# Optimization experiments

Hardware: AMD Instinct MI355X
Metric: run time of the kernel (lower is better)

The kernel has to match this reference:

```python
import jax, jax.numpy as jnp
import numpy as np

N, D_IN, D_K = 8192, 512, 64


def setup_inputs() -> dict:
    key = jax.random.key(0)
    k0, k1, k2, k3 = jax.random.split(key, 4)
    return {
        "inputs": jax.random.normal(k0, (N, D_IN), dtype=jnp.float32),
        "Wq": jax.random.normal(k1, (D_K, D_IN), dtype=jnp.float32),
        "Wk": jax.random.normal(k2, (D_K, D_IN), dtype=jnp.float32),
        "Wv": jax.random.normal(k3, (D_K, D_IN), dtype=jnp.float32),
    }


def reference(inputs, Wq, Wk, Wv):
    # nn.Linear(bias=False): x @ W.T, W has shape [out, in]
    q = inputs @ Wq.T  # [N, Dk]
    k = inputs @ Wk.T  # [N, Dk]
    v = inputs @ Wv.T  # [N, Dk]
    scaled = (q @ k.T) / jnp.sqrt(jnp.float32(D_K))  # [N, N]
    attn = jax.nn.softmax(scaled, axis=1)            # softmax over keys (dim=1)
    # weighted = values[:,None] * attn.T[:,:,None]; sum over dim 0 == attn @ v
    return attn @ v  # [N, Dk]
```

## Files before the change

### kernel.cpp

```cpp
#include <hip/hip_runtime.h>
#include <hip/hip_bf16.h>


#define N_TOK 8192
#define D_INN 512
#define DK    64

typedef __attribute__((ext_vector_type(8))) short bf16x8;
typedef __attribute__((ext_vector_type(4))) float f32x4;

#define GLOAD_LDS16(gsrc, ldst) \
  __builtin_amdgcn_global_load_lds( \
      (const __attribute__((address_space(1))) unsigned int*)(gsrc), \
      (__attribute__((address_space(3))) unsigned int*)(ldst), 16, 0, 0)

static __device__ __forceinline__ unsigned f2bf_u(float f) {
  union { float f; unsigned u; } v; v.f = f;
  return (v.u + 0x7FFFu + ((v.u >> 16) & 1u)) >> 16;
}
static __device__ __forceinline__ unsigned short f2bf(float f) { return (unsigned short)f2bf_u(f); }
static __device__ __forceinline__ float bf2f(unsigned short h) {
  union { unsigned u; float f; } v; v.u = ((unsigned)h) << 16; return v.f;
}
static __device__ __forceinline__ unsigned truncpk(float a, float b) {
  union { float f; unsigned u; } x, y; x.f = a; y.f = b;
  return (x.u >> 16) | (y.u & 0xFFFF0000u);
}
static __device__ __forceinline__ void split2(float a, float b, unsigned& hi, unsigned& lo) {
  unsigned ha = f2bf_u(a), hb = f2bf_u(b);
  float ra = a - bf2f((unsigned short)ha);
  float rb = b - bf2f((unsigned short)hb);
  hi = ha | (hb << 16);
  lo = f2bf_u(ra) | (f2bf_u(rb) << 16);
}
static __device__ __forceinline__ void split8(const float* p, bf16x8& hi, bf16x8& lo) {
  float4 a = *(const float4*)p;
  float4 b = *(const float4*)(p + 4);
  union { unsigned u[4]; bf16x8 v; } H, L;
  split2(a.x, a.y, H.u[0], L.u[0]);
  split2(a.z, a.w, H.u[1], L.u[1]);
  split2(b.x, b.y, H.u[2], L.u[2]);
  split2(b.z, b.w, H.u[3], L.u[3]);
  hi = H.v; lo = L.v;
}
static __device__ __forceinline__ bf16x8 round8(const float* p) {
  float4 a = *(const float4*)p;
  float4 b = *(const float4*)(p + 4);
  union { unsigned u[4]; bf16x8 v; } H;
  H.u[0] = f2bf_u(a.x) | (f2bf_u(a.y) << 16);
  H.u[1] = f2bf_u(a.z) | (f2bf_u(a.w) << 16);
  H.u[2] = f2bf_u(b.x) | (f2bf_u(b.y) << 16);
  H.u[3] = f2bf_u(b.z) | (f2bf_u(b.w) << 16);
  return H.v;
}

__global__ __launch_bounds__(256, 2) void qkv3(
    const float* __restrict__ X,
    const float* __restrict__ Wq, const float* __restrict__ Wk, const float* __restrict__ Wv,
    unsigned short* __restrict__ qhp, unsigned short* __restrict__ qlp,
    unsigned short* __restrict__ kph, unsigned short* __restrict__ kpl,
    unsigned short* __restrict__ vp) {
  const int tid = threadIdx.x, w = tid >> 6, l = tid & 63;
  const int l15 = l & 15, g = l >> 4;
  const int t0 = blockIdx.x * 16;
  const int dq = w * 16;

  f32x4 aq = {0.f, 0.f, 0.f, 0.f}, ak = aq, av = aq;

  for (int kc = 0; kc < D_INN; kc += 32) {
    bf16x8 ah, al;
    split8(X + (t0 + l15) * D_INN + kc + g * 8, ah, al);

    const int woff = (dq + l15) * D_INN + kc + g * 8;
    bf16x8 bqh, bql, bkh, bkl;
    split8(Wq + woff, bqh, bql);
    split8(Wk + woff, bkh, bkl);
    bf16x8 bvh = round8(Wv + woff);

    aq = __builtin_amdgcn_mfma_f32_16x16x32_bf16(ah, bqh, aq, 0, 0, 0);
    aq = __builtin_amdgcn_mfma_f32_16x16x32_bf16(ah, bql, aq, 0, 0, 0);
    aq = __builtin_amdgcn_mfma_f32_16x16x32_bf16(al, bqh, aq, 0, 0, 0);
    ak = __builtin_amdgcn_mfma_f32_16x16x32_bf16(ah, bkh, ak, 0, 0, 0);
    ak = __builtin_amdgcn_mfma_f32_16x16x32_bf16(ah, bkl, ak, 0, 0, 0);
    ak = __builtin_amdgcn_mfma_f32_16x16x32_bf16(al, bkh, ak, 0, 0, 0);
    av = __builtin_amdgcn_mfma_f32_16x16x32_bf16(ah, bvh, av, 0, 0, 0);
    av = __builtin_amdgcn_mfma_f32_16x16x32_bf16(al, bvh, av, 0, 0, 0);
  }

#pragma unroll
  for (int r = 0; r < 4; r++) {
    float v = aq[r] * 0.125f;
    int row = t0 + g * 4 + r;
    unsigned short h = f2bf(v);
    qhp[row * DK + dq + l15] = h;
    qlp[row * DK + dq + l15] = f2bf(v - bf2f(h));
  }
#pragma unroll
  for (int r = 0; r < 4; r++) {
    float v = ak[r];
    int t = t0 + g * 4 + r;
    int d = dq + l15;
    int off = (t >> 5) * 2048 + ((t >> 4) & 1) * 1024 + (d >> 5) * 512 +
              ((t & 15) + (((d >> 3) & 3) << 4)) * 8 + (d & 7);
    unsigned short h = f2bf(v);
    kph[off] = h;
    kpl[off] = f2bf(v - bf2f(h));
  }
  {
    int tg = t0 + g * 4;
    int d = dq + l15;
    int off = (tg >> 5) * 2048 + (d >> 4) * 512 +
              (((d & 15) + (((tg >> 3) & 3) << 4))) * 8 + (tg & 7);
    uint2 pk;
    pk.x = f2bf_u(av[0]) | (f2bf_u(av[1]) << 16);
    pk.y = f2bf_u(av[2]) | (f2bf_u(av[3]) << 16);
    *(uint2*)(vp + off) = pk;
  }
}

static __device__ __forceinline__ void stage_tile(
    const unsigned short* __restrict__ kph, const unsigned short* __restrict__ kpl,
    const unsigned short* __restrict__ vp, int kti,
    unsigned short* lds, int w, int l) {
  const unsigned short* kb = kph + kti * 2048;
  const unsigned short* lb = kpl + kti * 2048;
  const unsigned short* vb = vp + kti * 2048;
#pragma unroll
  for (int j = 0; j < 6; ++j) {
    int chunk = w * 6 + j;
    const unsigned short* src = (chunk < 8) ? kb : ((chunk < 16) ? lb : vb);
    GLOAD_LDS16(src + (chunk & 7) * 512 + l * 8, lds + chunk * 512);
  }
}

__global__ __launch_bounds__(256, 2) void attn5(
    const unsigned short* __restrict__ qhp, const unsigned short* __restrict__ qlp,
    const unsigned short* __restrict__ kph, const unsigned short* __restrict__ kpl,
    const unsigned short* __restrict__ vp,
    unsigned short* __restrict__ pnb, float* __restrict__ pden, float* __restrict__ pM) {
  __shared__ unsigned short kv_lds[2 * 12288];
  __shared__ unsigned short P_lds[4 * 16 * 72];

  const int tid = threadIdx.x, w = tid >> 6, l = tid & 63;
  const int l15 = l & 15, g = l >> 4;
  const int qblk = blockIdx.x >> 4, ks = blockIdx.x & 15;
  const int wq0 = qblk * 128 + w * 32;

  bf16x8 qhf[2][2], qlf[2][2];
#pragma unroll
  for (int u = 0; u < 2; u++)
#pragma unroll
    for (int c = 0; c < 2; c++) {
      int row = wq0 + u * 16 + l15;
      qhf[u][c] = *(const bf16x8*)(qhp + row * DK + c * 32 + g * 8);
      qlf[u][c] = *(const bf16x8*)(qlp + row * DK + c * 32 + g * 8);
    }

  const short onec = (short)0x3F80;
  const bf16x8 ones = {onec, onec, onec, onec, onec, onec, onec, onec};

  f32x4 accO[2][4], accL[2];
  float m[2] = {-1e30f, -1e30f};
#pragma unroll
  for (int u = 0; u < 2; u++) {
    accL[u] = f32x4{0.f, 0.f, 0.f, 0.f};
#pragma unroll
    for (int ds = 0; ds < 4; ds++) accO[u][ds] = f32x4{0.f, 0.f, 0.f, 0.f};
  }

  const int kti0 = ks * 16;
  stage_tile(kph, kpl, vp, kti0, kv_lds, w, l);
  __syncthreads();

  for (int t = 0; t < 8; ++t) {
    const int cb = (t & 1) ? 12288 : 0;
    const int pb = 12288 - cb;
    const int ktin = (t < 7) ? (kti0 + 2 * t + 2) : (kti0 + 2 * t);
    stage_tile(kph, kpl, vp, ktin, kv_lds + pb, w, l);

    const unsigned short* Kh = kv_lds + cb;
    const unsigned short* Kl = Kh + 4096;
    const unsigned short* Vv = Kh + 8192;

    f32x4 st[2][4];
#pragma unroll
    for (int s = 0; s < 4; s++) {
      bf16x8 khf[2], klf[2];
#pragma unroll
      for (int c = 0; c < 2; c++) {
        const int off = (s >> 1) * 2048 + (s & 1) * 1024 + c * 512 + l * 8;
        khf[c] = *(const bf16x8*)(Kh + off);
        klf[c] = *(const bf16x8*)(Kl + off);
      }
      __builtin_amdgcn_s_setprio(1);
#pragma unroll
      for (int u = 0; u < 2; u++) {
        f32x4 sa = {0.f, 0.f, 0.f, 0.f};
        sa = __builtin_amdgcn_mfma_f32_16x16x32_bf16(khf[0], qhf[u][0], sa, 0, 0, 0);
        sa = __builtin_amdgcn_mfma_f32_16x16x32_bf16(khf[1], qhf[u][1], sa, 0, 0, 0);
        sa = __builtin_amdgcn_mfma_f32_16x16x32_bf16(khf[0], qlf[u][0], sa, 0, 0, 0);
        sa = __builtin_amdgcn_mfma_f32_16x16x32_bf16(khf[1], qlf[u][1], sa, 0, 0, 0);
        sa = __builtin_amdgcn_mfma_f32_16x16x32_bf16(klf[0], qhf[u][0], sa, 0, 0, 0);
        sa = __builtin_amdgcn_mfma_f32_16x16x32_bf16(klf[1], qhf[u][1], sa, 0, 0, 0);
        st[u][s] = sa;
      }
      __builtin_amdgcn_s_setprio(0);
    }

    bf16x8 pa[2][2];
#pragma unroll
    for (int u = 0; u < 2; u++) {
      float t0m = fmaxf(fmaxf(st[u][0][0], st[u][0][1]), fmaxf(st[u][0][2], st[u][0][3]));
      float t1m = fmaxf(fmaxf(st[u][1][0], st[u][1][1]), fmaxf(st[u][1][2], st[u][1][3]));
      float t2m = fmaxf(fmaxf(st[u][2][0], st[u][2][1]), fmaxf(st[u][2][2], st[u][2][3]));
      float t3m = fmaxf(fmaxf(st[u][3][0], st[u][3][1]), fmaxf(st[u][3][2], st[u][3][3]));
      float tm = fmaxf(fmaxf(t0m, t1m), fmaxf(t2m, t3m));
      tm = fmaxf(tm, __shfl_xor(tm, 16, 64));
      tm = fmaxf(tm, __shfl_xor(tm, 32, 64));
      if (__any(tm > m[u] + 8.f)) {
        float mn = fmaxf(m[u], tm);
        float fac = __expf(m[u] - mn);
        m[u] = mn;
#pragma unroll
        for (int r = 0; r < 4; r++) {
          float fr = __shfl(fac, g * 4 + r, 64);
          accL[u][r] *= fr;
#pragma unroll
          for (int ds = 0; ds < 4; ds++) accO[u][ds][r] *= fr;
        }
      }
      const int base = (w * 16 + l15) * 72;
#pragma unroll
      for (int s = 0; s < 4; s++) {
        float p0 = __expf(st[u][s][0] - m[u]);
        float p1 = __expf(st[u][s][1] - m[u]);
        float p2 = __expf(st[u][s][2] - m[u]);
        float p3 = __expf(st[u][s][3] - m[u]);
        *(unsigned*)&P_lds[base + s * 16 + g * 4]     = truncpk(p0, p1);
        *(unsigned*)&P_lds[base + s * 16 + g * 4 + 2] = truncpk(p2, p3);
      }
#pragma unroll
      for (int c = 0; c < 2; c++)
        pa[u][c] = *(const bf16x8*)&P_lds[base + c * 32 + g * 8];
      accL[u] = __builtin_amdgcn_mfma_f32_16x16x32_bf16(pa[u][0], ones, accL[u], 0, 0, 0);
      accL[u] = __builtin_amdgcn_mfma_f32_16x16x32_bf16(pa[u][1], ones, accL[u], 0, 0, 0);
    }

    __builtin_amdgcn_s_setprio(1);
#pragma unroll
    for (int ds = 0; ds < 4; ds++) {
      bf16x8 vb[2];
#pragma unroll
      for (int c = 0; c < 2; c++)
        vb[c] = *(const bf16x8*)(Vv + c * 2048 + ds * 512 + l * 8);
#pragma unroll
      for (int u = 0; u < 2; u++) {
        accO[u][ds] = __builtin_amdgcn_mfma_f32_16x16x32_bf16(pa[u][0], vb[0], accO[u][ds], 0, 0, 0);
        accO[u][ds] = __builtin_amdgcn_mfma_f32_16x16x32_bf16(pa[u][1], vb[1], accO[u][ds], 0, 0, 0);
      }
    }
    __builtin_amdgcn_s_setprio(0);

    __syncthreads();
  }

#pragma unroll
  for (int u = 0; u < 2; u++) {
#pragma unroll
    for (int ds = 0; ds < 4; ds++)
#pragma unroll
      for (int r = 0; r < 4; r++)
        pnb[(size_t)ks * (N_TOK * DK) + (wq0 + u * 16 + g * 4 + r) * DK + ds * 16 + l15] =
            f2bf(accO[u][ds][r]);
    if (l15 == 0) {
#pragma unroll
      for (int r = 0; r < 4; r++) pden[ks * N_TOK + wq0 + u * 16 + g * 4 + r] = accL[u][r];
    }
    if (g == 0) pM[ks * N_TOK + wq0 + u * 16 + l15] = m[u];
  }
}

__global__ __launch_bounds__(256) void merge16(
    const unsigned short* __restrict__ pnb, const float* __restrict__ pden,
    const float* __restrict__ pM, float* __restrict__ out) {
  int i = blockIdx.x * 256 + threadIdx.x;
  int q = i >> 6, d = i & 63;
  float M = -1e30f;
#pragma unroll
  for (int s = 0; s < 16; s++) M = fmaxf(M, pM[s * N_TOK + q]);
  float num = 0.f, den = 0.f;
#pragma unroll
  for (int s = 0; s < 16; s++) {
    float e = __expf(pM[s * N_TOK + q] - M);
    num += bf2f(pnb[(size_t)s * (N_TOK * DK) + q * DK + d]) * e;
    den += pden[s * N_TOK + q] * e;
  }
  out[i] = num / den;
}

extern "C" void kernel_launch(void* const* d_in, const int* in_sizes, int n_in,
                              void* d_out, int out_size, void* d_ws, size_t ws_size,
                              hipStream_t stream) {
  (void)in_sizes; (void)n_in; (void)out_size; (void)ws_size;
  const float* X  = (const float*)d_in[0];
  const float* Wq = (const float*)d_in[1];
  const float* Wk = (const float*)d_in[2];
  const float* Wv = (const float*)d_in[3];

  char* base = (char*)d_ws;
  unsigned short* pnb = (unsigned short*)(base);
  unsigned short* qhp = (unsigned short*)(base + 16777216);
  unsigned short* qlp = (unsigned short*)(base + 17825792);
  unsigned short* kph = (unsigned short*)(base + 18874368);
  unsigned short* kpl = (unsigned short*)(base + 19922944);
  unsigned short* vp  = (unsigned short*)(base + 20971520);
  float* pden = (float*)(base + 22020096);
  float* pM   = (float*)(base + 22544384);

  qkv3<<<N_TOK / 16, 256, 0, stream>>>(X, Wq, Wk, Wv, qhp, qlp, kph, kpl, vp);
  attn5<<<1024, 256, 0, stream>>>(qhp, qlp, kph, kpl, vp, pnb, pden, pM);
  merge16<<<(N_TOK * DK) / 256, 256, 0, stream>>>(pnb, pden, pM, (float*)d_out);
}
```

Before: 149.3 us.

## Halve key splits, fold log2e into Q scale, interleave PV MFMAs per row group

The flash-attention split-K factor drops from 16 to 8, so each block walks twice as many key tiles and the merge kernel reads half as many partial results. The 1/sqrt(d)·log2(e) factor is folded into the Q scaling so exp2f can replace __expf in the softmax and merge. The rescale threshold is widened to match the base-2 scale. V fragments are loaded once per tile ahead of the softmax, and the PV MFMAs are issued per row group right after its P is written. This cuts partial-output traffic and merge work, but with 512 blocks there is less parallelism to fill the GPU.

Measured after the change: 151.6 us. Within noise of the previous version (+1.6%).

```diff
diff --git a/kernel.cpp b/kernel.cpp
--- a/kernel.cpp
+++ b/kernel.cpp
@@ -5,6 +5,7 @@
 #define N_TOK 8192
 #define D_INN 512
 #define DK    64
+#define QSCALE 0.18033688011112042f
 
 typedef __attribute__((ext_vector_type(8))) short bf16x8;
 typedef __attribute__((ext_vector_type(4))) float f32x4;
@@ -89,7 +90,7 @@
 
 #pragma unroll
   for (int r = 0; r < 4; r++) {
-    float v = aq[r] * 0.125f;
+    float v = aq[r] * QSCALE;
     int row = t0 + g * 4 + r;
     unsigned short h = f2bf(v);
     qhp[row * DK + dq + l15] = h;
@@ -133,7 +134,7 @@
   }
 }
 
-__global__ __launch_bounds__(256, 2) void attn5(
+__global__ __launch_bounds__(256, 2) void attn6(
     const unsigned short* __restrict__ qhp, const unsigned short* __restrict__ qlp,
     const unsigned short* __restrict__ kph, const unsigned short* __restrict__ kpl,
     const unsigned short* __restrict__ vp,
@@ -143,7 +144,7 @@
 
   const int tid = threadIdx.x, w = tid >> 6, l = tid & 63;
   const int l15 = l & 15, g = l >> 4;
-  const int qblk = blockIdx.x >> 4, ks = blockIdx.x & 15;
+  const int qblk = blockIdx.x >> 3, ks = blockIdx.x & 7;
   const int wq0 = qblk * 128 + w * 32;
 
   bf16x8 qhf[2][2], qlf[2][2];
@@ -168,14 +169,14 @@
     for (int ds = 0; ds < 4; ds++) accO[u][ds] = f32x4{0.f, 0.f, 0.f, 0.f};
   }
 
-  const int kti0 = ks * 16;
+  const int kti0 = ks * 32;
   stage_tile(kph, kpl, vp, kti0, kv_lds, w, l);
   __syncthreads();
 
-  for (int t = 0; t < 8; ++t) {
+  for (int t = 0; t < 16; ++t) {
     const int cb = (t & 1) ? 12288 : 0;
     const int pb = 12288 - cb;
-    const int ktin = (t < 7) ? (kti0 + 2 * t + 2) : (kti0 + 2 * t);
+    const int ktin = (t < 15) ? (kti0 + 2 * t + 2) : (kti0 + 2 * t);
     stage_tile(kph, kpl, vp, ktin, kv_lds + pb, w, l);
 
     const unsigned short* Kh = kv_lds + cb;
@@ -207,7 +208,13 @@
       __builtin_amdgcn_s_setprio(0);
     }
 
-    bf16x8 pa[2][2];
+    bf16x8 vb[4][2];
+#pragma unroll
+    for (int ds = 0; ds < 4; ds++)
+#pragma unroll
+      for (int c = 0; c < 2; c++)
+        vb[ds][c] = *(const bf16x8*)(Vv + c * 2048 + ds * 512 + l * 8);
+
 #pragma unroll
     for (int u = 0; u < 2; u++) {
       float t0m = fmaxf(fmaxf(st[u][0][0], st[u][0][1]), fmaxf(st[u][0][2], st[u][0][3]));
@@ -217,9 +224,9 @@
       float tm = fmaxf(fmaxf(t0m, t1m), fmaxf(t2m, t3m));
       tm = fmaxf(tm, __shfl_xor(tm, 16, 64));
       tm = fmaxf(tm, __shfl_xor(tm, 32, 64));
-      if (__any(tm > m[u] + 8.f)) {
+      if (__any(tm > m[u] + 11.0f)) {
         float mn = fmaxf(m[u], tm);
-        float fac = __expf(m[u] - mn);
+        float fac = exp2f(m[u] - mn);
         m[u] = mn;
 #pragma unroll
         for (int r = 0; r < 4; r++) {
@@ -232,34 +239,25 @@
       const int base = (w * 16 + l15) * 72;
 #pragma unroll
       for (int s = 0; s < 4; s++) {
-        float p0 = __expf(st[u][s][0] - m[u]);
-        float p1 = __expf(st[u][s][1] - m[u]);
-        float p2 = __expf(st[u][s][2] - m[u]);
-        float p3 = __expf(st[u][s][3] - m[u]);
+        float p0 = exp2f(st[u][s][0] - m[u]);
+        float p1 = exp2f(st[u][s][1] - m[u]);
+        float p2 = exp2f(st[u][s][2] - m[u]);
+        float p3 = exp2f(st[u][s][3] - m[u]);
         *(unsigned*)&P_lds[base + s * 16 + g * 4]     = truncpk(p0, p1);
         *(unsigned*)&P_lds[base + s * 16 + g * 4 + 2] = truncpk(p2, p3);
       }
-#pragma unroll
-      for (int c = 0; c < 2; c++)
-        pa[u][c] = *(const bf16x8*)&P_lds[base + c * 32 + g * 8];
-      accL[u] = __builtin_amdgcn_mfma_f32_16x16x32_bf16(pa[u][0], ones, accL[u], 0, 0, 0);
-      accL[u] = __builtin_amdgcn_mfma_f32_16x16x32_bf16(pa[u][1], ones, accL[u], 0, 0, 0);
+      bf16x8 pa0 = *(const bf16x8*)&P_lds[base + g * 8];
+      bf16x8 pa1 = *(const bf16x8*)&P_lds[base + 32 + g * 8];
+      __builtin_amdgcn_s_setprio(1);
+      accL[u] = __builtin_amdgcn_mfma_f32_16x16x32_bf16(pa0, ones, accL[u], 0, 0, 0);
+      accL[u] = __builtin_amdgcn_mfma_f32_16x16x32_bf16(pa1, ones, accL[u], 0, 0, 0);
+#pragma unroll
+      for (int ds = 0; ds < 4; ds++) {
+        accO[u][ds] = __builtin_amdgcn_mfma_f32_16x16x32_bf16(pa0, vb[ds][0], accO[u][ds], 0, 0, 0);
+        accO[u][ds] = __builtin_amdgcn_mfma_f32_16x16x32_bf16(pa1, vb[ds][1], accO[u][ds], 0, 0, 0);
+      }
+      __builtin_amdgcn_s_setprio(0);
     }
-
-    __builtin_amdgcn_s_setprio(1);
-#pragma unroll
-    for (int ds = 0; ds < 4; ds++) {
-      bf16x8 vb[2];
-#pragma unroll
-      for (int c = 0; c < 2; c++)
-        vb[c] = *(const bf16x8*)(Vv + c * 2048 + ds * 512 + l * 8);
-#pragma unroll
-      for (int u = 0; u < 2; u++) {
-        accO[u][ds] = __builtin_amdgcn_mfma_f32_16x16x32_bf16(pa[u][0], vb[0], accO[u][ds], 0, 0, 0);
-        accO[u][ds] = __builtin_amdgcn_mfma_f32_16x16x32_bf16(pa[u][1], vb[1], accO[u][ds], 0, 0, 0);
-      }
-    }
-    __builtin_amdgcn_s_setprio(0);
 
     __syncthreads();
   }
@@ -280,18 +278,18 @@
   }
 }
 
-__global__ __launch_bounds__(256) void merge16(
+__global__ __launch_bounds__(256) void merge8(
     const unsigned short* __restrict__ pnb, const float* __restrict__ pden,
     const float* __restrict__ pM, float* __restrict__ out) {
   int i = blockIdx.x * 256 + threadIdx.x;
   int q = i >> 6, d = i & 63;
   float M = -1e30f;
 #pragma unroll
-  for (int s = 0; s < 16; s++) M = fmaxf(M, pM[s * N_TOK + q]);
+  for (int s = 0; s < 8; s++) M = fmaxf(M, pM[s * N_TOK + q]);
   float num = 0.f, den = 0.f;
 #pragma unroll
-  for (int s = 0; s < 16; s++) {
-    float e = __expf(pM[s * N_TOK + q] - M);
+  for (int s = 0; s < 8; s++) {
+    float e = exp2f(pM[s * N_TOK + q] - M);
     num += bf2f(pnb[(size_t)s * (N_TOK * DK) + q * DK + d]) * e;
     den += pden[s * N_TOK + q] * e;
   }
@@ -318,6 +316,6 @@
   float* pM   = (float*)(base + 22544384);
 
   qkv3<<<N_TOK / 16, 256, 0, stream>>>(X, Wq, Wk, Wv, qhp, qlp, kph, kpl, vp);
-  attn5<<<1024, 256, 0, stream>>>(qhp, qlp, kph, kpl, vp, pnb, pden, pM);
-  merge16<<<(N_TOK * DK) / 256, 256, 0, stream>>>(pnb, pden, pM, (float*)d_out);
-}
+  attn6<<<512, 256, 0, stream>>>(qhp, qlp, kph, kpl, vp, pnb, pden, pM);
+  merge8<<<(N_TOK * DK) / 256, 256, 0, stream>>>(pnb, pden, pM, (float*)d_out);
+}
```
